# Optimization experiments

Hardware: AMD Instinct MI355X
Metric: run time of the kernel (lower is better)

The kernel has to match this reference:

```python
import jax, jax.numpy as jnp
import numpy as np

B, S, H = 32, 4096, 512


def setup_inputs() -> dict:
    key = jax.random.key(0)
    ks = jax.random.split(key, 8)
    scale = 1.0 / np.sqrt(H)
    return {
        "query": jax.random.normal(ks[0], (B, H), dtype=jnp.float32),
        "keys": jax.random.normal(ks[1], (B, S, 2 * H), dtype=jnp.float32),
        "Wa_w": jax.random.uniform(ks[2], (H, H), jnp.float32, -scale, scale),
        "Wa_b": jax.random.uniform(ks[3], (H,), jnp.float32, -scale, scale),
        "Ua_w": jax.random.uniform(ks[4], (H, 2 * H), jnp.float32, -scale, scale),
        "Ua_b": jax.random.uniform(ks[5], (H,), jnp.float32, -scale, scale),
        "Va_w": jax.random.uniform(ks[6], (1, H), jnp.float32, -scale, scale),
        "Va_b": jax.random.uniform(ks[7], (1,), jnp.float32, -scale, scale),
    }


def reference(query, keys, Wa_w, Wa_b, Ua_w, Ua_b, Va_w, Va_b):
    # query: [B,H], keys: [B,S,2H]
    q_proj = query @ Wa_w.T + Wa_b                       # [B,H]
    k_proj = jnp.einsum('bsk,hk->bsh', keys, Ua_w) + Ua_b  # [B,S,H]
    energy = jnp.tanh(q_proj[:, None, :] + k_proj)        # [B,S,H]
    scores = jnp.einsum('bsh,h->bs', energy, Va_w[0]) + Va_b[0]  # [B,S]
    attn_weights = jax.nn.softmax(scores, axis=1)         # [B,S]
    context = jnp.einsum('bs,bsk->bk', attn_weights, keys)  # [B,2H]
    return (context, attn_weights)
```

## Files before the change

### kernel.cpp

```cpp
#include <hip/hip_runtime.h>
#include <hip/hip_bf16.h>
#include <cstdint>
#include <cstddef>

#define NB 32
#define NS 4096
#define NH 512
#define NK 1024

typedef __attribute__((ext_vector_type(8))) short short8;
typedef __attribute__((ext_vector_type(4))) float f32x4;

#define SB() __builtin_amdgcn_sched_barrier(0)
#define LGKM0() asm volatile("s_waitcnt lgkmcnt(0)" ::: "memory")
#define VM0() asm volatile("s_waitcnt vmcnt(0)" ::: "memory")
#define BAR() __builtin_amdgcn_s_barrier()

__device__ __forceinline__ unsigned short f2bf_s(float f) {
  union { float f; unsigned u; } x; x.f = f;
  unsigned r = x.u + 0x7fffu + ((x.u >> 16) & 1u);
  return (unsigned short)(r >> 16);
}

__device__ __forceinline__ unsigned pk2(float lo, float hi) {
  __hip_bfloat162 h = __float22bfloat162_rn(float2{lo, hi});
  union { __hip_bfloat162 h; unsigned u; } c; c.h = h;
  return c.u;
}

__device__ __forceinline__ void gload16(const void* g, void* l) {
  __builtin_amdgcn_global_load_lds(
      (const __attribute__((address_space(1))) unsigned int*)g,
      (__attribute__((address_space(3))) unsigned int*)l, 16, 0, 0);
}

__global__ void k_ua_pack(const float* __restrict__ ua, unsigned short* __restrict__ out) {
  int t = blockIdx.x * 256 + threadIdx.x;
  int c = t & 2047;
  int kc = (t >> 11) & 15;
  int bn = t >> 15;
  int nloc = c >> 3;
  int k16 = (c & 7) ^ (nloc & 7);
  const float* src = ua + (size_t)(bn * 256 + nloc) * NK + kc * 64 + k16 * 8;
  float4 a = *(const float4*)src;
  float4 b2 = *(const float4*)(src + 4);
  ushort4 o0, o1;
  o0.x = f2bf_s(a.x);  o0.y = f2bf_s(a.y);  o0.z = f2bf_s(a.z);  o0.w = f2bf_s(a.w);
  o1.x = f2bf_s(b2.x); o1.y = f2bf_s(b2.y); o1.z = f2bf_s(b2.z); o1.w = f2bf_s(b2.w);
  ushort4* dst = (ushort4*)(out + (size_t)t * 8);
  dst[0] = o0; dst[1] = o1;
}

__global__ void k_qproj(const float* __restrict__ q, const float* __restrict__ ww,
                        const float* __restrict__ wb, const float* __restrict__ ub,
                        float* __restrict__ qp) {
  int b = blockIdx.y;
  int h = blockIdx.x * 128 + threadIdx.x;
  const float* qr = q + b * NH;
  const float* wr = ww + h * NH;
  float acc = 0.f;
  for (int k = 0; k < NH; k += 4) {
    float4 a = *(const float4*)(qr + k);
    float4 c = *(const float4*)(wr + k);
    acc += a.x * c.x + a.y * c.y + a.z * c.z + a.w * c.w;
  }
  qp[b * NH + h] = acc + wb[h] + ub[h];
}

__global__ __launch_bounds__(512, 2)
void k_scores7(const float* __restrict__ keys, const unsigned short* __restrict__ uapk,
               const float* __restrict__ qproj, const float* __restrict__ vaw,
               float* __restrict__ scores_part) {
  __shared__ alignas(16) unsigned short Albuf[2][256 * 64];
  __shared__ alignas(16) unsigned short Blbuf[2][256 * 64];
  __shared__ float qp_s[256];
  __shared__ float va_s[256];
  __shared__ float red[256][4];

  const int sblk = blockIdx.x;
  const int bn   = blockIdx.y;
  const int b    = blockIdx.z;
  const int tid  = threadIdx.x;
  const int w    = tid >> 6;
  const int l    = tid & 63;
  const int rg   = w >> 2;
  const int cg   = w & 3;
  const int l15  = l & 15;
  const int lq   = l >> 4;
  const int asw  = (l15 & 7) << 4;

  if (tid < 256) {
    qp_s[tid] = qproj[b * NH + bn * 256 + tid];
    va_s[tid] = vaw[bn * 256 + tid];
  }

  const int srow = tid >> 1;
  const int skh  = tid & 1;
  const float* agbase = keys + ((size_t)b * NS + sblk * 256 + srow) * NK + skh * 32;
  const int wsw = (srow & 7) << 4;

  const char* bgbase = (const char*)uapk + (size_t)bn * 524288 + w * 4096 + l * 16;

  f32x4 acc[8][4];
  #pragma unroll
  for (int i = 0; i < 8; ++i)
    #pragma unroll
    for (int j = 0; j < 4; ++j)
      acc[i][j] = (f32x4){0.f, 0.f, 0.f, 0.f};

  float4 ca0, ca1, ca2, ca3, ca4, ca5, ca6, ca7;

  ca0 = *(const float4*)(agbase + 0);
  ca1 = *(const float4*)(agbase + 4);
  ca2 = *(const float4*)(agbase + 8);
  ca3 = *(const float4*)(agbase + 12);
  ca4 = *(const float4*)(agbase + 16);
  ca5 = *(const float4*)(agbase + 20);
  ca6 = *(const float4*)(agbase + 24);
  ca7 = *(const float4*)(agbase + 28);
  #pragma unroll
  for (int j2 = 0; j2 < 4; ++j2)
    gload16(bgbase + j2 * 1024, (char*)&Blbuf[0][0] + w * 4096 + j2 * 1024);
  {
    char* Aw = (char*)&Albuf[0][0] + srow * 128;
    uint4 q0, q1, q2, q3;
    q0.x = pk2(ca0.x, ca0.y); q0.y = pk2(ca0.z, ca0.w);
    q0.z = pk2(ca1.x, ca1.y); q0.w = pk2(ca1.z, ca1.w);
    q1.x = pk2(ca2.x, ca2.y); q1.y = pk2(ca2.z, ca2.w);
    q1.z = pk2(ca3.x, ca3.y); q1.w = pk2(ca3.z, ca3.w);
    q2.x = pk2(ca4.x, ca4.y); q2.y = pk2(ca4.z, ca4.w);
    q2.z = pk2(ca5.x, ca5.y); q2.w = pk2(ca5.z, ca5.w);
    q3.x = pk2(ca6.x, ca6.y); q3.y = pk2(ca6.z, ca6.w);
    q3.z = pk2(ca7.x, ca7.y); q3.w = pk2(ca7.z, ca7.w);
    *(uint4*)(Aw + ((skh * 64 +  0) ^ wsw)) = q0;
    *(uint4*)(Aw + ((skh * 64 + 16) ^ wsw)) = q1;
    *(uint4*)(Aw + ((skh * 64 + 32) ^ wsw)) = q2;
    *(uint4*)(Aw + ((skh * 64 + 48) ^ wsw)) = q3;
  }
  VM0();
  LGKM0();
  SB();
  BAR();

  for (int kc = 0; kc < 16; ++kc) {
    const int cur = kc & 1;
    const char* Ab = (const char*)&Albuf[cur][0];
    const char* Bb = (const char*)&Blbuf[cur][0];
    char* Aw = (char*)&Albuf[cur ^ 1][0] + srow * 128;
    const bool stg = (kc < 15);
    short8 bf[4], af[4];

    #pragma unroll
    for (int ct = 0; ct < 4; ++ct)
      bf[ct] = *(const short8*)(Bb + (cg * 64 + ct * 16 + l15) * 128 + ((lq * 16) ^ asw));
    #pragma unroll
    for (int r4 = 0; r4 < 4; ++r4)
      af[r4] = *(const short8*)(Ab + (rg * 128 + r4 * 16 + l15) * 128 + ((lq * 16) ^ asw));
    if (stg) {
      const float* ag = agbase + (kc + 1) * 64;
      ca0 = *(const float4*)(ag + 0);
      ca1 = *(const float4*)(ag + 4);
      ca2 = *(const float4*)(ag + 8);
      ca3 = *(const float4*)(ag + 12);
    }
    SB(); BAR(); LGKM0(); SB();
    __builtin_amdgcn_s_setprio(1);
    #pragma unroll
    for (int r4 = 0; r4 < 4; ++r4)
      #pragma unroll
      for (int ct = 0; ct < 4; ++ct)
        acc[r4][ct] = __builtin_amdgcn_mfma_f32_16x16x32_bf16(af[r4], bf[ct], acc[r4][ct], 0, 0, 0);
    __builtin_amdgcn_s_setprio(0);
    SB(); BAR();

    #pragma unroll
    for (int r4 = 0; r4 < 4; ++r4)
      af[r4] = *(const short8*)(Ab + (rg * 128 + (4 + r4) * 16 + l15) * 128 + ((lq * 16) ^ asw));
    if (stg) {
      const float* ag = agbase + (kc + 1) * 64;
      ca4 = *(const float4*)(ag + 16);
      ca5 = *(const float4*)(ag + 20);
      ca6 = *(const float4*)(ag + 24);
      ca7 = *(const float4*)(ag + 28);
    }
    SB(); BAR(); LGKM0(); SB();
    __builtin_amdgcn_s_setprio(1);
    #pragma unroll
    for (int r4 = 0; r4 < 4; ++r4)
      #pragma unroll
      for (int ct = 0; ct < 4; ++ct)
        acc[4 + r4][ct] = __builtin_amdgcn_mfma_f32_16x16x32_bf16(af[r4], bf[ct], acc[4 + r4][ct], 0, 0, 0);
    __builtin_amdgcn_s_setprio(0);
    SB(); BAR();

    #pragma unroll
    for (int ct = 0; ct < 4; ++ct)
      bf[ct] = *(const short8*)(Bb + (cg * 64 + ct * 16 + l15) * 128 + ((64 + lq * 16) ^ asw));
    #pragma unroll
    for (int r4 = 0; r4 < 4; ++r4)
      af[r4] = *(const short8*)(Ab + (rg * 128 + r4 * 16 + l15) * 128 + ((64 + lq * 16) ^ asw));
    if (stg) {
      const char* bg = bgbase + (size_t)(kc + 1) * 32768;
      #pragma unroll
      for (int j2 = 0; j2 < 4; ++j2)
        gload16(bg + j2 * 1024, (char*)&Blbuf[cur ^ 1][0] + w * 4096 + j2 * 1024);
    }
    SB(); BAR(); LGKM0(); SB();
    __builtin_amdgcn_s_setprio(1);
    #pragma unroll
    for (int r4 = 0; r4 < 4; ++r4)
      #pragma unroll
      for (int ct = 0; ct < 4; ++ct)
        acc[r4][ct] = __builtin_amdgcn_mfma_f32_16x16x32_bf16(af[r4], bf[ct], acc[r4][ct], 0, 0, 0);
    __builtin_amdgcn_s_setprio(0);
    SB(); BAR();

    #pragma unroll
    for (int r4 = 0; r4 < 4; ++r4)
      af[r4] = *(const short8*)(Ab + (rg * 128 + (4 + r4) * 16 + l15) * 128 + ((64 + lq * 16) ^ asw));
    if (stg) {
      uint4 q0, q1, q2, q3;
      q0.x = pk2(ca0.x, ca0.y); q0.y = pk2(ca0.z, ca0.w);
      q0.z = pk2(ca1.x, ca1.y); q0.w = pk2(ca1.z, ca1.w);
      q1.x = pk2(ca2.x, ca2.y); q1.y = pk2(ca2.z, ca2.w);
      q1.z = pk2(ca3.x, ca3.y); q1.w = pk2(ca3.z, ca3.w);
      q2.x = pk2(ca4.x, ca4.y); q2.y = pk2(ca4.z, ca4.w);
      q2.z = pk2(ca5.x, ca5.y); q2.w = pk2(ca5.z, ca5.w);
      q3.x = pk2(ca6.x, ca6.y); q3.y = pk2(ca6.z, ca6.w);
      q3.z = pk2(ca7.x, ca7.y); q3.w = pk2(ca7.z, ca7.w);
      *(uint4*)(Aw + ((skh * 64 +  0) ^ wsw)) = q0;
      *(uint4*)(Aw + ((skh * 64 + 16) ^ wsw)) = q1;
      *(uint4*)(Aw + ((skh * 64 + 32) ^ wsw)) = q2;
      *(uint4*)(Aw + ((skh * 64 + 48) ^ wsw)) = q3;
      VM0();
    }
    LGKM0();
    SB(); BAR(); LGKM0(); SB();
    __builtin_amdgcn_s_setprio(1);
    #pragma unroll
    for (int r4 = 0; r4 < 4; ++r4)
      #pragma unroll
      for (int ct = 0; ct < 4; ++ct)
        acc[4 + r4][ct] = __builtin_amdgcn_mfma_f32_16x16x32_bf16(af[r4], bf[ct], acc[4 + r4][ct], 0, 0, 0);
    __builtin_amdgcn_s_setprio(0);
    SB(); BAR();
  }

  #pragma unroll
  for (int rt = 0; rt < 8; ++rt) {
    #pragma unroll
    for (int reg = 0; reg < 4; ++reg) {
      float sum = 0.f;
      #pragma unroll
      for (int ct = 0; ct < 4; ++ct) {
        int gn = cg * 64 + ct * 16 + l15;
        float x = qp_s[gn] + acc[rt][ct][reg];
        float e = __expf(2.f * x);
        float th = 1.f - __fdividef(2.f, e + 1.f);
        sum += va_s[gn] * th;
      }
      sum += __shfl_xor(sum, 1);
      sum += __shfl_xor(sum, 2);
      sum += __shfl_xor(sum, 4);
      sum += __shfl_xor(sum, 8);
      if (l15 == 0)
        red[rg * 128 + rt * 16 + lq * 4 + reg][cg] = sum;
    }
  }
  __syncthreads();
  if (tid < 256) {
    float s = red[tid][0] + red[tid][1] + red[tid][2] + red[tid][3];
    scores_part[((size_t)bn * NB + b) * NS + sblk * 256 + tid] = s;
  }
}

__global__ void k_softmax(const float* __restrict__ sp, const float* __restrict__ vab,
                          float* __restrict__ attn) {
  __shared__ float redm[4];
  __shared__ float reds[4];
  int b = blockIdx.x, tid = threadIdx.x;
  const float* r0 = sp + (size_t)b * NS;
  const float* r1 = sp + (size_t)(NB + b) * NS;
  float vb = vab[0];
  float v[16];
  float m = -1e30f;
  #pragma unroll
  for (int i = 0; i < 16; ++i) {
    int idx = i * 256 + tid;
    v[i] = r0[idx] + r1[idx] + vb;
    m = fmaxf(m, v[i]);
  }
  #pragma unroll
  for (int off = 1; off < 64; off <<= 1) m = fmaxf(m, __shfl_xor(m, off));
  if ((tid & 63) == 0) redm[tid >> 6] = m;
  __syncthreads();
  m = fmaxf(fmaxf(redm[0], redm[1]), fmaxf(redm[2], redm[3]));
  float s = 0.f;
  #pragma unroll
  for (int i = 0; i < 16; ++i) { v[i] = expf(v[i] - m); s += v[i]; }
  #pragma unroll
  for (int off = 1; off < 64; off <<= 1) s += __shfl_xor(s, off);
  if ((tid & 63) == 0) reds[tid >> 6] = s;
  __syncthreads();
  s = reds[0] + reds[1] + reds[2] + reds[3];
  float inv = 1.f / s;
  float* o = attn + (size_t)b * NS;
  #pragma unroll
  for (int i = 0; i < 16; ++i) o[i * 256 + tid] = v[i] * inv;
}

__global__ void k_ctx_partial(const float* __restrict__ keys, const float* __restrict__ attn,
                              float* __restrict__ part) {
  __shared__ float w_s[512];
  int b = blockIdx.y, seg = blockIdx.x, tid = threadIdx.x;
  int sbeg = seg * 512;
  w_s[tid] = attn[(size_t)b * NS + sbeg + tid];
  w_s[tid + 256] = attn[(size_t)b * NS + sbeg + 256 + tid];
  __syncthreads();
  const float* kp = keys + ((size_t)b * NS + sbeg) * NK + tid * 4;
  float ax = 0.f, ay = 0.f, az = 0.f, aw = 0.f;
  #pragma unroll 4
  for (int s = 0; s < 512; ++s) {
    float4 kv = *(const float4*)(kp + (size_t)s * NK);
    float wv = w_s[s];
    ax += wv * kv.x; ay += wv * kv.y; az += wv * kv.z; aw += wv * kv.w;
  }
  float4 o; o.x = ax; o.y = ay; o.z = az; o.w = aw;
  *(float4*)(part + ((size_t)(seg * NB + b) << 10) + tid * 4) = o;
}

__global__ void k_ctx_reduce(const float* __restrict__ part, float* __restrict__ ctx) {
  int i = blockIdx.x * 256 + threadIdx.x;
  int b = i >> 10, c = i & 1023;
  float s = 0.f;
  #pragma unroll
  for (int seg = 0; seg < 8; ++seg) s += part[((size_t)(seg * NB + b) << 10) + c];
  ctx[i] = s;
}

extern "C" void kernel_launch(void* const* d_in, const int* in_sizes, int n_in,
                              void* d_out, int out_size, void* d_ws, size_t ws_size,
                              hipStream_t stream) {
  const float* query = (const float*)d_in[0];
  const float* keys  = (const float*)d_in[1];
  const float* Wa_w  = (const float*)d_in[2];
  const float* Wa_b  = (const float*)d_in[3];
  const float* Ua_w  = (const float*)d_in[4];
  const float* Ua_b  = (const float*)d_in[5];
  const float* Va_w  = (const float*)d_in[6];
  const float* Va_b  = (const float*)d_in[7];

  float* out      = (float*)d_out;
  float* ctx_out  = out;
  float* attn_out = out + NB * NK;

  unsigned short* ua_pk = (unsigned short*)d_ws;
  float* qproj  = (float*)((char*)d_ws + (1u << 20));
  float* spart  = (float*)((char*)d_ws + (1u << 20) + (1u << 16));
  float* part   = (float*)((char*)d_ws + (2u << 20) + (1u << 16));

  k_ua_pack<<<256, 256, 0, stream>>>(Ua_w, ua_pk);
  k_qproj<<<dim3(4, NB), 128, 0, stream>>>(query, Wa_w, Wa_b, Ua_b, qproj);
  k_scores7<<<dim3(16, 2, NB), 512, 0, stream>>>(keys, ua_pk, qproj, Va_w, spart);
  k_softmax<<<NB, 256, 0, stream>>>(spart, Va_b, attn_out);
  k_ctx_partial<<<dim3(8, NB), 256, 0, stream>>>(keys, attn_out, part);
  k_ctx_reduce<<<NB * NK / 256, 256, 0, stream>>>(part, ctx_out);
}
```

Before: 442.3 us.

## Pre-pack keys to swizzled bf16 and stream them via direct global-to-LDS loads

Adds a kernel that converts the fp32 keys into a swizzled bf16 tile layout in workspace. A new scores kernel then loads both the A (keys) and B (Ua) tiles with the same direct 16-byte global-to-LDS loads, removing the in-loop fp32 register staging and bf16 packing. The goal is a simpler, more asynchronous main loop. In exchange it adds a full pass over the keys (read fp32, write bf16) and needs a 256 MB workspace. The new path only runs when the workspace is large enough; otherwise the old kernel is used. Launch bounds also drop to one block per SIMD.

Result: no change. 439.7 us (-0.6%).

```diff
diff --git a/kernel.cpp b/kernel.cpp
--- a/kernel.cpp
+++ b/kernel.cpp
@@ -51,6 +51,22 @@
   dst[0] = o0; dst[1] = o1;
 }
 
+__global__ void k_keys_pack(const float* __restrict__ keys, unsigned short* __restrict__ out) {
+  size_t t = (size_t)blockIdx.x * 256 + threadIdx.x;
+  int c    = (int)(t & 2047);
+  int kc   = (int)((t >> 11) & 15);
+  int sb   = (int)(t >> 15);
+  int nloc = c >> 3;
+  int k16  = (c & 7) ^ (nloc & 7);
+  const float* src = keys + ((size_t)sb * 256 + nloc) * NK + kc * 64 + k16 * 8;
+  float4 a  = *(const float4*)src;
+  float4 b2 = *(const float4*)(src + 4);
+  uint4 o;
+  o.x = pk2(a.x, a.y);  o.y = pk2(a.z, a.w);
+  o.z = pk2(b2.x, b2.y); o.w = pk2(b2.z, b2.w);
+  *(uint4*)(out + t * 8) = o;
+}
+
 __global__ void k_qproj(const float* __restrict__ q, const float* __restrict__ ww,
                         const float* __restrict__ wb, const float* __restrict__ ub,
                         float* __restrict__ qp) {
@@ -67,8 +83,8 @@
   qp[b * NH + h] = acc + wb[h] + ub[h];
 }
 
-__global__ __launch_bounds__(512, 2)
-void k_scores7(const float* __restrict__ keys, const unsigned short* __restrict__ uapk,
+__global__ __launch_bounds__(512, 1)
+void k_scores8(const unsigned short* __restrict__ keyspk, const unsigned short* __restrict__ uapk,
                const float* __restrict__ qproj, const float* __restrict__ vaw,
                float* __restrict__ scores_part) {
   __shared__ alignas(16) unsigned short Albuf[2][256 * 64];
@@ -94,30 +110,165 @@
     va_s[tid] = vaw[bn * 256 + tid];
   }
 
-  const int srow = tid >> 1;
-  const int skh  = tid & 1;
+  const char* agbase = (const char*)keyspk + ((size_t)(b * 16 + sblk)) * 524288 + w * 4096 + l * 16;
+  const char* bgbase = (const char*)uapk + (size_t)bn * 524288 + w * 4096 + l * 16;
+
+  f32x4 acc[8][4];
+  #pragma unroll
+  for (int i = 0; i < 8; ++i)
+    #pragma unroll
+    for (int j = 0; j < 4; ++j)
+      acc[i][j] = (f32x4){0.f, 0.f, 0.f, 0.f};
+
+  #pragma unroll
+  for (int j2 = 0; j2 < 4; ++j2)
+    gload16(agbase + j2 * 1024, (char*)&Albuf[0][0] + w * 4096 + j2 * 1024);
+  #pragma unroll
+  for (int j2 = 0; j2 < 4; ++j2)
+    gload16(bgbase + j2 * 1024, (char*)&Blbuf[0][0] + w * 4096 + j2 * 1024);
+  VM0();
+  LGKM0();
+  SB();
+  BAR();
+
+  for (int kc = 0; kc < 16; ++kc) {
+    const int cur = kc & 1;
+    const char* Ab = (const char*)&Albuf[cur][0];
+    const char* Bb = (const char*)&Blbuf[cur][0];
+    const bool stg = (kc < 15);
+    short8 bf[4], af[4];
+
+    #pragma unroll
+    for (int ct = 0; ct < 4; ++ct)
+      bf[ct] = *(const short8*)(Bb + (cg * 64 + ct * 16 + l15) * 128 + ((lq * 16) ^ asw));
+    #pragma unroll
+    for (int r4 = 0; r4 < 4; ++r4)
+      af[r4] = *(const short8*)(Ab + (rg * 128 + r4 * 16 + l15) * 128 + ((lq * 16) ^ asw));
+    if (stg) {
+      const char* ag = agbase + (size_t)(kc + 1) * 32768;
+      #pragma unroll
+      for (int j2 = 0; j2 < 4; ++j2)
+        gload16(ag + j2 * 1024, (char*)&Albuf[cur ^ 1][0] + w * 4096 + j2 * 1024);
+    }
+    SB(); BAR(); LGKM0(); SB();
+    __builtin_amdgcn_s_setprio(1);
+    #pragma unroll
+    for (int r4 = 0; r4 < 4; ++r4)
+      #pragma unroll
+      for (int ct = 0; ct < 4; ++ct)
+        acc[r4][ct] = __builtin_amdgcn_mfma_f32_16x16x32_bf16(af[r4], bf[ct], acc[r4][ct], 0, 0, 0);
+    __builtin_amdgcn_s_setprio(0);
+    SB(); BAR();
+
+    #pragma unroll
+    for (int r4 = 0; r4 < 4; ++r4)
+      af[r4] = *(const short8*)(Ab + (rg * 128 + (4 + r4) * 16 + l15) * 128 + ((lq * 16) ^ asw));
+    if (stg) {
+      const char* bg = bgbase + (size_t)(kc + 1) * 32768;
+      #pragma unroll
+      for (int j2 = 0; j2 < 4; ++j2)
+        gload16(bg + j2 * 1024, (char*)&Blbuf[cur ^ 1][0] + w * 4096 + j2 * 1024);
+    }
+    SB(); BAR(); LGKM0(); SB();
+    __builtin_amdgcn_s_setprio(1);
+    #pragma unroll
+    for (int r4 = 0; r4 < 4; ++r4)
+      #pragma unroll
+      for (int ct = 0; ct < 4; ++ct)
+        acc[4 + r4][ct] = __builtin_amdgcn_mfma_f32_16x16x32_bf16(af[r4], bf[ct], acc[4 + r4][ct], 0, 0, 0);
+    __builtin_amdgcn_s_setprio(0);
+    SB(); BAR();
+
+    #pragma unroll
+    for (int ct = 0; ct < 4; ++ct)
+      bf[ct] = *(const short8*)(Bb + (cg * 64 + ct * 16 + l15) * 128 + ((64 + lq * 16) ^ asw));
+    #pragma unroll
+    for (int r4 = 0; r4 < 4; ++r4)
+      af[r4] = *(const short8*)(Ab + (rg * 128 + r4 * 16 + l15) * 128 + ((64 + lq * 16) ^ asw));
+    SB(); BAR(); LGKM0(); SB();
+    __builtin_amdgcn_s_setprio(1);
+    #pragma unroll
+    for (int r4 = 0; r4 < 4; ++r4)
+      #pragma unroll
+      for (int ct = 0; ct < 4; ++ct)
+        acc[r4][ct] = __builtin_amdgcn_mfma_f32_16x16x32_bf16(af[r4], bf[ct], acc[r4][ct], 0, 0, 0);
+    __builtin_amdgcn_s_setprio(0);
+    SB(); BAR();
+
+    #pragma unroll
+    for (int r4 = 0; r4 < 4; ++r4)
+      af[r4] = *(const short8*)(Ab + (rg * 128 + (4 + r4) * 16 + l15) * 128 + ((64 + lq * 16) ^ asw));
+    if (stg) VM0();
+    SB(); BAR(); LGKM0(); SB();
+    __builtin_amdgcn_s_setprio(1);
+    #pragma unroll
+    for (int r4 = 0; r4 < 4; ++r4)
+      #pragma unroll
+      for (int ct = 0; ct < 4; ++ct)
+        acc[4 + r4][ct] = __builtin_amdgcn_mfma_f32_16x16x32_bf16(af[r4], bf[ct], acc[4 + r4][ct], 0, 0, 0);
+    __builtin_amdgcn_s_setprio(0);
+    SB(); BAR();
+  }
+
+  #pragma unroll
+  for (int rt = 0; rt < 8; ++rt) {
+    #pragma unroll
+    for (int reg = 0; reg < 4; ++reg) {
+      float sum = 0.f;
+      #pragma unroll
+      for (int ct = 0; ct < 4; ++ct) {
+        int gn = cg * 64 + ct * 16 + l15;
+        float x = qp_s[gn] + acc[rt][ct][reg];
+        float e = __expf(2.f * x);
+        float th = 1.f - __fdividef(2.f, e + 1.f);
+        sum += va_s[gn] * th;
+      }
+      sum += __shfl_xor(sum, 1);
+      sum += __shfl_xor(sum, 2);
+      sum += __shfl_xor(sum, 4);
+      sum += __shfl_xor(sum, 8);
+      if (l15 == 0)
+        red[rg * 128 + rt * 16 + lq * 4 + reg][cg] = sum;
+    }
+  }
+  __syncthreads();
+  if (tid < 256) {
+    float s = red[tid][0] + red[tid][1] + red[tid][2] + red[tid][3];
+    scores_part[((size_t)bn * NB + b) * NS + sblk * 256 + tid] = s;
+  }
+}
+
+__global__ __launch_bounds__(512, 2)
+void k_scores7(const float* __restrict__ keys, const unsigned short* __restrict__ uapk,
+               const float* __restrict__ qproj, const float* __restrict__ vaw,
+               float* __restrict__ scores_part) {
+  __shared__ alignas(16) unsigned short Albuf[2][256 * 64];
+  __shared__ alignas(16) unsigned short Blbuf[2][256 * 64];
+  __shared__ float qp_s[256];
+  __shared__ float va_s[256];
+  __shared__ float red[256][4];
+  const int sblk = blockIdx.x, bn = blockIdx.y, b = blockIdx.z;
+  const int tid = threadIdx.x, w = tid >> 6, l = tid & 63;
+  const int rg = w >> 2, cg = w & 3, l15 = l & 15, lq = l >> 4;
+  const int asw = (l15 & 7) << 4;
+  if (tid < 256) {
+    qp_s[tid] = qproj[b * NH + bn * 256 + tid];
+    va_s[tid] = vaw[bn * 256 + tid];
+  }
+  const int srow = tid >> 1, skh = tid & 1;
   const float* agbase = keys + ((size_t)b * NS + sblk * 256 + srow) * NK + skh * 32;
   const int wsw = (srow & 7) << 4;
-
   const char* bgbase = (const char*)uapk + (size_t)bn * 524288 + w * 4096 + l * 16;
-
   f32x4 acc[8][4];
   #pragma unroll
   for (int i = 0; i < 8; ++i)
     #pragma unroll
-    for (int j = 0; j < 4; ++j)
-      acc[i][j] = (f32x4){0.f, 0.f, 0.f, 0.f};
-
+    for (int j = 0; j < 4; ++j) acc[i][j] = (f32x4){0.f, 0.f, 0.f, 0.f};
   float4 ca0, ca1, ca2, ca3, ca4, ca5, ca6, ca7;
-
-  ca0 = *(const float4*)(agbase + 0);
-  ca1 = *(const float4*)(agbase + 4);
-  ca2 = *(const float4*)(agbase + 8);
-  ca3 = *(const float4*)(agbase + 12);
-  ca4 = *(const float4*)(agbase + 16);
-  ca5 = *(const float4*)(agbase + 20);
-  ca6 = *(const float4*)(agbase + 24);
-  ca7 = *(const float4*)(agbase + 28);
+  ca0 = *(const float4*)(agbase + 0);  ca1 = *(const float4*)(agbase + 4);
+  ca2 = *(const float4*)(agbase + 8);  ca3 = *(const float4*)(agbase + 12);
+  ca4 = *(const float4*)(agbase + 16); ca5 = *(const float4*)(agbase + 20);
+  ca6 = *(const float4*)(agbase + 24); ca7 = *(const float4*)(agbase + 28);
   #pragma unroll
   for (int j2 = 0; j2 < 4; ++j2)
     gload16(bgbase + j2 * 1024, (char*)&Blbuf[0][0] + w * 4096 + j2 * 1024);
@@ -137,11 +288,7 @@
     *(uint4*)(Aw + ((skh * 64 + 32) ^ wsw)) = q2;
     *(uint4*)(Aw + ((skh * 64 + 48) ^ wsw)) = q3;
   }
-  VM0();
-  LGKM0();
-  SB();
-  BAR();
-
+  VM0(); LGKM0(); SB(); BAR();
   for (int kc = 0; kc < 16; ++kc) {
     const int cur = kc & 1;
     const char* Ab = (const char*)&Albuf[cur][0];
@@ -149,7 +296,6 @@
     char* Aw = (char*)&Albuf[cur ^ 1][0] + srow * 128;
     const bool stg = (kc < 15);
     short8 bf[4], af[4];
-
     #pragma unroll
     for (int ct = 0; ct < 4; ++ct)
       bf[ct] = *(const short8*)(Bb + (cg * 64 + ct * 16 + l15) * 128 + ((lq * 16) ^ asw));
@@ -158,10 +304,8 @@
       af[r4] = *(const short8*)(Ab + (rg * 128 + r4 * 16 + l15) * 128 + ((lq * 16) ^ asw));
     if (stg) {
       const float* ag = agbase + (kc + 1) * 64;
-      ca0 = *(const float4*)(ag + 0);
-      ca1 = *(const float4*)(ag + 4);
-      ca2 = *(const float4*)(ag + 8);
-      ca3 = *(const float4*)(ag + 12);
+      ca0 = *(const float4*)(ag + 0);  ca1 = *(const float4*)(ag + 4);
+      ca2 = *(const float4*)(ag + 8);  ca3 = *(const float4*)(ag + 12);
     }
     SB(); BAR(); LGKM0(); SB();
     __builtin_amdgcn_s_setprio(1);
@@ -172,16 +316,13 @@
         acc[r4][ct] = __builtin_amdgcn_mfma_f32_16x16x32_bf16(af[r4], bf[ct], acc[r4][ct], 0, 0, 0);
     __builtin_amdgcn_s_setprio(0);
     SB(); BAR();
-
     #pragma unroll
     for (int r4 = 0; r4 < 4; ++r4)
       af[r4] = *(const short8*)(Ab + (rg * 128 + (4 + r4) * 16 + l15) * 128 + ((lq * 16) ^ asw));
     if (stg) {
       const float* ag = agbase + (kc + 1) * 64;
-      ca4 = *(const float4*)(ag + 16);
-      ca5 = *(const float4*)(ag + 20);
-      ca6 = *(const float4*)(ag + 24);
-      ca7 = *(const float4*)(ag + 28);
+      ca4 = *(const float4*)(ag + 16); ca5 = *(const float4*)(ag + 20);
+      ca6 = *(const float4*)(ag + 24); ca7 = *(const float4*)(ag + 28);
     }
     SB(); BAR(); LGKM0(); SB();
     __builtin_amdgcn_s_setprio(1);
@@ -192,7 +333,6 @@
         acc[4 + r4][ct] = __builtin_amdgcn_mfma_f32_16x16x32_bf16(af[r4], bf[ct], acc[4 + r4][ct], 0, 0, 0);
     __builtin_amdgcn_s_setprio(0);
     SB(); BAR();
-
     #pragma unroll
     for (int ct = 0; ct < 4; ++ct)
       bf[ct] = *(const short8*)(Bb + (cg * 64 + ct * 16 + l15) * 128 + ((64 + lq * 16) ^ asw));
@@ -214,7 +354,6 @@
         acc[r4][ct] = __builtin_amdgcn_mfma_f32_16x16x32_bf16(af[r4], bf[ct], acc[r4][ct], 0, 0, 0);
     __builtin_amdgcn_s_setprio(0);
     SB(); BAR();
-
     #pragma unroll
     for (int r4 = 0; r4 < 4; ++r4)
       af[r4] = *(const short8*)(Ab + (rg * 128 + (4 + r4) * 16 + l15) * 128 + ((64 + lq * 16) ^ asw));
@@ -245,7 +384,6 @@
     __builtin_amdgcn_s_setprio(0);
     SB(); BAR();
   }
-
   #pragma unroll
   for (int rt = 0; rt < 8; ++rt) {
     #pragma unroll
@@ -263,8 +401,7 @@
       sum += __shfl_xor(sum, 2);
       sum += __shfl_xor(sum, 4);
       sum += __shfl_xor(sum, 8);
-      if (l15 == 0)
-        red[rg * 128 + rt * 16 + lq * 4 + reg][cg] = sum;
+      if (l15 == 0) red[rg * 128 + rt * 16 + lq * 4 + reg][cg] = sum;
     }
   }
   __syncthreads();
@@ -358,10 +495,18 @@
   float* qproj  = (float*)((char*)d_ws + (1u << 20));
   float* spart  = (float*)((char*)d_ws + (1u << 20) + (1u << 16));
   float* part   = (float*)((char*)d_ws + (2u << 20) + (1u << 16));
+  unsigned short* keys_pk = (unsigned short*)((char*)d_ws + (4u << 20));
+
+  const size_t need = (4ull << 20) + 268435456ull;
 
   k_ua_pack<<<256, 256, 0, stream>>>(Ua_w, ua_pk);
   k_qproj<<<dim3(4, NB), 128, 0, stream>>>(query, Wa_w, Wa_b, Ua_b, qproj);
-  k_scores7<<<dim3(16, 2, NB), 512, 0, stream>>>(keys, ua_pk, qproj, Va_w, spart);
+  if (ws_size >= need) {
+    k_keys_pack<<<65536, 256, 0, stream>>>(keys, keys_pk);
+    k_scores8<<<dim3(16, 2, NB), 512, 0, stream>>>(keys_pk, ua_pk, qproj, Va_w, spart);
+  } else {
+    k_scores7<<<dim3(16, 2, NB), 512, 0, stream>>>(keys, ua_pk, qproj, Va_w, spart);
+  }
   k_softmax<<<NB, 256, 0, stream>>>(spart, Va_b, attn_out);
   k_ctx_partial<<<dim3(8, NB), 256, 0, stream>>>(keys, attn_out, part);
   k_ctx_reduce<<<NB * NK / 256, 256, 0, stream>>>(part, ctx_out);
```
